# Optimization experiments

Hardware: AMD Instinct MI355X
Metric: run time of the kernel (lower is better)

The kernel has to match this reference:

```python
import jax, jax.numpy as jnp
import numpy as np

CUTOFF = 5.0  # init kwarg
KEEP_LOOPS = False  # init kwarg


def setup_inputs() -> dict:
    key = jax.random.key(0)
    B, n = 64, 512
    # scale so distances span the cutoff=5.0 shell (nontrivial mask)
    positions = jax.random.normal(key, (B * n, 3), dtype=jnp.float32) * 6.0
    num_nodes = jnp.full((B,), n, dtype=jnp.int32)
    return {"num_nodes": num_nodes, "positions": positions}


def reference(num_nodes, positions):
    """connected_within_cutoff with equal-size graphs, static shapes.

    Returns (edge_index_all, edge_mask, num_edges, distances):
      edge_index_all: [B*n*n, 2] int32 global node indices of all candidate pairs
      edge_mask:      [B*n*n]   bool, True where pair is a kept edge
                      (dist <= cutoff, no self loops). edge_index_all[edge_mask]
                      equals the torch module's edge_index.
      num_edges:      [B] int32 kept edges per graph
      distances:      [B, n, n] float32 pairwise distances (float output)
    """
    B = num_nodes.shape[0]
    n = positions.shape[0] // B
    pos = positions.reshape(B, n, 3)

    # pairwise distances per graph: [B, n, n]
    diff = pos[:, :, None, :] - pos[:, None, :, :]
    dist = jnp.sqrt(jnp.sum(diff * diff, axis=-1))

    mask = dist <= CUTOFF
    if not KEEP_LOOPS:
        mask = mask & ~jnp.eye(n, dtype=bool)[None]

    num_edges = jnp.sum(mask, axis=(1, 2)).astype(jnp.int32)

    # candidate edge_index with per-graph offsets
    idx = jnp.arange(n, dtype=jnp.int32)
    src = jnp.broadcast_to(idx[:, None], (n, n))  # row index (argwhere order)
    dst = jnp.broadcast_to(idx[None, :], (n, n))
    pairs = jnp.stack([src, dst], axis=-1)  # [n, n, 2]
    offsets = (jnp.arange(B, dtype=jnp.int32) * n)[:, None, None, None]
    edge_index_all = (pairs[None] + offsets).reshape(-1, 2)  # [B*n*n, 2]

    return edge_index_all, mask.reshape(-1), num_edges, dist
```

## Files before the change

### kernel.cpp

```cpp
#include <hip/hip_runtime.h>


__global__ void zero_counts_kernel(float* __restrict__ ne, int B) {
    int t = blockIdx.x * blockDim.x + threadIdx.x;
    if (t < B) ne[t] = 0.0f;
}

__global__ __launch_bounds__(256) void cwc_kernel(
    const float* __restrict__ pos,
    float* __restrict__ ei,
    float* __restrict__ maskout,
    float* __restrict__ numedges,
    float* __restrict__ distout,
    int n)
{
    extern __shared__ float spos[];
    const int ROWS = 16;
    const int bpg  = n / ROWS;
    const int b    = blockIdx.x / bpg;
    const int r0   = (blockIdx.x - b * bpg) * ROWS;
    const int nf   = n * 3;

    const float* gp = pos + (long long)b * nf;
    for (int idx = threadIdx.x; idx < nf; idx += blockDim.x)
        spos[idx] = gp[idx];
    __syncthreads();

    const int tid  = threadIdx.x;
    const int tpr  = n / 4;
    const int half = tid / tpr;
    const int jj0  = (tid - half * tpr) * 4;

    float4 q0 = *(const float4*)(spos + 3 * jj0);
    float4 q1 = *(const float4*)(spos + 3 * jj0 + 4);
    float4 q2 = *(const float4*)(spos + 3 * jj0 + 8);
    const float qx[4] = {q0.x, q0.w, q1.z, q2.y};
    const float qy[4] = {q0.y, q1.x, q1.w, q2.z};
    const float qz[4] = {q0.z, q1.y, q2.x, q2.w};

    const int gb = b * n;
    const long long pairbase = (long long)(gb + r0) * n;

    int cnt = 0;
#pragma unroll
    for (int k = 0; k < 8; ++k) {
        const int i = r0 + 2 * k + half;
        const float px = spos[3 * i], py = spos[3 * i + 1], pz = spos[3 * i + 2];
        float d[4], m[4];
#pragma unroll
        for (int jj = 0; jj < 4; ++jj) {
            float dx = px - qx[jj];
            float dy = py - qy[jj];
            float dz = pz - qz[jj];
            float dd = sqrtf(fmaf(dx, dx, fmaf(dy, dy, dz * dz)));
            d[jj] = dd;
            bool keep = (dd <= 5.0f) && ((jj0 + jj) != i);
            m[jj] = keep ? 1.0f : 0.0f;
            cnt += keep ? 1 : 0;
        }
        const long long o = pairbase + (long long)(2 * k + half) * n + jj0;
        *(float4*)(distout + o) = float4{d[0], d[1], d[2], d[3]};
        *(float4*)(maskout + o) = float4{m[0], m[1], m[2], m[3]};
    }

    float4* eib = (float4*)(ei + 2 * pairbase);
    const float gj0 = (float)(gb + 2 * tid);
#pragma unroll
    for (int k2 = 0; k2 < ROWS; ++k2) {
        const float gif = (float)(gb + r0 + k2);
        eib[k2 * 256 + tid] = float4{gif, gj0, gif, gj0 + 1.0f};
    }

#pragma unroll
    for (int off = 32; off > 0; off >>= 1)
        cnt += __shfl_down(cnt, off, 64);
    __shared__ int wsum[4];
    const int wave = tid >> 6;
    if ((tid & 63) == 0) wsum[wave] = cnt;
    __syncthreads();
    if (tid == 0) {
        int s = wsum[0] + wsum[1] + wsum[2] + wsum[3];
        atomicAdd(numedges + b, (float)s);
    }
}

extern "C" void kernel_launch(void* const* d_in, const int* in_sizes, int n_in,
                              void* d_out, int out_size, void* d_ws, size_t ws_size,
                              hipStream_t stream) {
    const float* pos = (const float*)d_in[1];
    const int B = in_sizes[0];
    const int total_nodes = in_sizes[1] / 3;
    const int n = total_nodes / B;

    const long long P = (long long)B * n * n;
    float* out      = (float*)d_out;
    float* ei       = out;
    float* maskout  = out + 2 * P;
    float* numedges = out + 3 * P;
    float* distout  = out + 3 * P + B;

    hipLaunchKernelGGL(zero_counts_kernel, dim3((B + 63) / 64), dim3(64), 0, stream,
                       numedges, B);

    const int ROWS = 16;
    const int nblocks = B * (n / ROWS);
    const size_t lds_bytes = (size_t)n * 3 * sizeof(float);

    hipLaunchKernelGGL(cwc_kernel, dim3(nblocks), dim3(256), lds_bytes, stream,
                       pos, ei, maskout, numedges, distout, n);
}
```

Before: 262.3 us.

## Use nontemporal stores, vectorized LDS fill, and partial-sum count reduction

All output writes (edge indices, distances, mask) now use nontemporal vector stores, and the edge-index writes move ahead of the position load so they can issue while the global load is in flight. The LDS fill uses float4 loads instead of scalar ones. Per-graph edge counts go to per-block partials in workspace and a small second kernel sums them, replacing the zeroing kernel and the float atomics. The kernel is write-bandwidth bound, so the aim is better streaming-store behaviour; the cost is an extra serial reduction launch.

```diff
diff --git a/kernel.cpp b/kernel.cpp
--- a/kernel.cpp
+++ b/kernel.cpp
@@ -1,17 +1,14 @@
 #include <hip/hip_runtime.h>
 
 
-__global__ void zero_counts_kernel(float* __restrict__ ne, int B) {
-    int t = blockIdx.x * blockDim.x + threadIdx.x;
-    if (t < B) ne[t] = 0.0f;
-}
+typedef float float4n __attribute__((ext_vector_type(4)));
 
 __global__ __launch_bounds__(256) void cwc_kernel(
     const float* __restrict__ pos,
     float* __restrict__ ei,
     float* __restrict__ maskout,
-    float* __restrict__ numedges,
     float* __restrict__ distout,
+    float* __restrict__ partials,
     int n)
 {
     extern __shared__ float spos[];
@@ -19,27 +16,36 @@
     const int bpg  = n / ROWS;
     const int b    = blockIdx.x / bpg;
     const int r0   = (blockIdx.x - b * bpg) * ROWS;
-    const int nf   = n * 3;
+    const int tid  = threadIdx.x;
+    const int gb   = b * n;
+    const long long pairbase = (long long)(gb + r0) * n;
 
-    const float* gp = pos + (long long)b * nf;
-    for (int idx = threadIdx.x; idx < nf; idx += blockDim.x)
-        spos[idx] = gp[idx];
+    float4n* eib = (float4n*)(ei + 2 * pairbase);
+    const float gj0 = (float)(gb + 2 * tid);
+#pragma unroll
+    for (int k2 = 0; k2 < ROWS; ++k2) {
+        const float gif = (float)(gb + r0 + k2);
+        __builtin_nontemporal_store(float4n{gif, gj0, gif, gj0 + 1.0f},
+                                    eib + k2 * 256 + tid);
+    }
+
+    const float4n* gp4 = (const float4n*)(pos + (long long)b * n * 3);
+    float4n* sp4 = (float4n*)spos;
+    const int nf4 = (n * 3) / 4;
+    for (int idx = tid; idx < nf4; idx += 256)
+        sp4[idx] = gp4[idx];
     __syncthreads();
 
-    const int tid  = threadIdx.x;
     const int tpr  = n / 4;
     const int half = tid / tpr;
     const int jj0  = (tid - half * tpr) * 4;
 
-    float4 q0 = *(const float4*)(spos + 3 * jj0);
-    float4 q1 = *(const float4*)(spos + 3 * jj0 + 4);
-    float4 q2 = *(const float4*)(spos + 3 * jj0 + 8);
+    float4n q0 = *(const float4n*)(spos + 3 * jj0);
+    float4n q1 = *(const float4n*)(spos + 3 * jj0 + 4);
+    float4n q2 = *(const float4n*)(spos + 3 * jj0 + 8);
     const float qx[4] = {q0.x, q0.w, q1.z, q2.y};
     const float qy[4] = {q0.y, q1.x, q1.w, q2.z};
     const float qz[4] = {q0.z, q1.y, q2.x, q2.w};
-
-    const int gb = b * n;
-    const long long pairbase = (long long)(gb + r0) * n;
 
     int cnt = 0;
 #pragma unroll
@@ -59,28 +65,31 @@
             cnt += keep ? 1 : 0;
         }
         const long long o = pairbase + (long long)(2 * k + half) * n + jj0;
-        *(float4*)(distout + o) = float4{d[0], d[1], d[2], d[3]};
-        *(float4*)(maskout + o) = float4{m[0], m[1], m[2], m[3]};
-    }
-
-    float4* eib = (float4*)(ei + 2 * pairbase);
-    const float gj0 = (float)(gb + 2 * tid);
-#pragma unroll
-    for (int k2 = 0; k2 < ROWS; ++k2) {
-        const float gif = (float)(gb + r0 + k2);
-        eib[k2 * 256 + tid] = float4{gif, gj0, gif, gj0 + 1.0f};
+        __builtin_nontemporal_store(float4n{d[0], d[1], d[2], d[3]},
+                                    (float4n*)(distout + o));
+        __builtin_nontemporal_store(float4n{m[0], m[1], m[2], m[3]},
+                                    (float4n*)(maskout + o));
     }
 
 #pragma unroll
     for (int off = 32; off > 0; off >>= 1)
         cnt += __shfl_down(cnt, off, 64);
     __shared__ int wsum[4];
-    const int wave = tid >> 6;
-    if ((tid & 63) == 0) wsum[wave] = cnt;
+    if ((tid & 63) == 0) wsum[tid >> 6] = cnt;
     __syncthreads();
-    if (tid == 0) {
-        int s = wsum[0] + wsum[1] + wsum[2] + wsum[3];
-        atomicAdd(numedges + b, (float)s);
+    if (tid == 0)
+        partials[blockIdx.x] = (float)(wsum[0] + wsum[1] + wsum[2] + wsum[3]);
+}
+
+__global__ void reduce_counts_kernel(const float* __restrict__ partials,
+                                     float* __restrict__ numedges,
+                                     int bpg, int B) {
+    int b = blockIdx.x * blockDim.x + threadIdx.x;
+    if (b < B) {
+        const float* p = partials + b * bpg;
+        float s = 0.0f;
+        for (int k = 0; k < bpg; ++k) s += p[k];
+        numedges[b] = s;
     }
 }
 
@@ -98,14 +107,15 @@
     float* maskout  = out + 2 * P;
     float* numedges = out + 3 * P;
     float* distout  = out + 3 * P + B;
-
-    hipLaunchKernelGGL(zero_counts_kernel, dim3((B + 63) / 64), dim3(64), 0, stream,
-                       numedges, B);
+    float* partials = (float*)d_ws;
 
     const int ROWS = 16;
-    const int nblocks = B * (n / ROWS);
+    const int bpg = n / ROWS;
+    const int nblocks = B * bpg;
     const size_t lds_bytes = (size_t)n * 3 * sizeof(float);
 
     hipLaunchKernelGGL(cwc_kernel, dim3(nblocks), dim3(256), lds_bytes, stream,
-                       pos, ei, maskout, numedges, distout, n);
+                       pos, ei, maskout, distout, partials, n);
+    hipLaunchKernelGGL(reduce_counts_kernel, dim3((B + 63) / 64), dim3(64), 0, stream,
+                       partials, numedges, bpg, B);
 }
```

Result: slower. 272.6 us (+3.9%).
